# Optimization experiments

Hardware: AMD Instinct MI355X
Metric: run time of the kernel (lower is better)

## Reference

```python
import jax, jax.numpy as jnp
import numpy as np


def setup_inputs() -> dict:
    key = jax.random.key(0)
    ks = jax.random.split(key, 5)
    B, S, E, H, D = 4, 2048, 1024, 16, 64
    sc = 1.0 / np.sqrt(E)
    x = jax.random.normal(ks[0], (B, S, E), dtype=jnp.float32)
    Wq = jax.random.normal(ks[1], (H, E, D), dtype=jnp.float32) * sc
    Wk = jax.random.normal(ks[2], (H, E, D), dtype=jnp.float32) * sc
    Wv = jax.random.normal(ks[3], (H, E, D), dtype=jnp.float32) * sc
    Wo = jax.random.normal(ks[4], (E, E), dtype=jnp.float32) * sc
    bo = jnp.zeros((E,), dtype=jnp.float32)
    return {"x": x, "Wq": Wq, "Wk": Wk, "Wv": Wv, "Wo": Wo, "bo": bo}


def reference(x, Wq, Wk, Wv, Wo, bo):
    # x: [B,S,E]; Wq/Wk/Wv: [H,E,D]; Wo: [E,E]; bo: [E]
    B, S, E = x.shape
    H, _, D = Wq.shape
    q = jnp.einsum('bse,hed->bhsd', x, Wq)
    k = jnp.einsum('bse,hed->bhsd', x, Wk)
    v = jnp.einsum('bse,hed->bhsd', x, Wv)
    scale = jnp.asarray(D, x.dtype) ** -0.5
    att = jnp.einsum('bhsd,bhtd->bhst', q, k) * scale  # [B,H,S,S]
    causal = jnp.tril(jnp.ones((S, S), dtype=bool))
    att = jnp.where(causal, att, jnp.asarray(-jnp.inf, att.dtype))
    att = jax.nn.softmax(att, axis=-1)
    out = jnp.einsum('bhst,bhtd->bhsd', att, v)  # [B,H,S,D]
    # concat heads in order (head dim-major on last axis), then project
    out = out.transpose(0, 2, 1, 3).reshape(B, S, H * D)
    return out @ Wo.T + bo
```

## Files before the change

kernel.cpp:

```cpp
#include <hip/hip_runtime.h>
#include <hip/hip_bf16.h>

#define BB 4
#define SS 2048
#define EE 1024
#define HH 16
#define DD 64
#define MM (BB*SS)
#define HD (HH*DD)
#define NQKV (3*HD)

typedef __bf16 bf16_t;
typedef __bf16 bf16x4 __attribute__((ext_vector_type(4)));
typedef __bf16 bf16x8 __attribute__((ext_vector_type(8)));
typedef float f32x4 __attribute__((ext_vector_type(4)));

#define MFMA16(a,b,c) __builtin_amdgcn_mfma_f32_16x16x32_bf16(a,b,c,0,0,0)
#define NEG_INF (-__builtin_huge_valf())
#define QSCALE 0.1803368801111204f

__device__ __forceinline__ void gload_lds16(const void* g, void* l) {
  __builtin_amdgcn_global_load_lds((const __attribute__((address_space(1))) unsigned int*)g,
                                   (__attribute__((address_space(3))) unsigned int*)l,
                                   16, 0, 0);
}

#define SBAR() __builtin_amdgcn_s_barrier()
#define SCHB() __builtin_amdgcn_sched_barrier(0)
#define VMCNT2 do { asm volatile("s_waitcnt vmcnt(2)" ::: "memory"); } while(0)
#define VMCNT0 do { asm volatile("s_waitcnt vmcnt(0)" ::: "memory"); } while(0)

__global__ __launch_bounds__(256)
void k_f32_to_bf16(const float* __restrict__ in, bf16_t* __restrict__ out, int n8) {
  int i = blockIdx.x*256 + threadIdx.x;
  if (i >= n8) return;
  const float4* p = reinterpret_cast<const float4*>(in) + (size_t)i*2;
  float4 a = p[0], b = p[1];
  bf16x8 o;
  o[0]=(bf16_t)a.x; o[1]=(bf16_t)a.y; o[2]=(bf16_t)a.z; o[3]=(bf16_t)a.w;
  o[4]=(bf16_t)b.x; o[5]=(bf16_t)b.y; o[6]=(bf16_t)b.z; o[7]=(bf16_t)b.w;
  *reinterpret_cast<bf16x8*>(out + (size_t)i*8) = o;
}

__global__ __launch_bounds__(256)
void k_conv_wqkv(const float* __restrict__ Wq, const float* __restrict__ Wk,
                 const float* __restrict__ Wv, bf16_t* __restrict__ Wt) {
  __shared__ float t[64][65];
  int wh = blockIdx.x;
  int which = wh >> 4, h = wh & 15;
  int e0 = blockIdx.y * 64;
  const float* W = (which==0) ? Wq : (which==1) ? Wk : Wv;
  const float* src = W + (size_t)h*EE*DD;
  int r = threadIdx.x >> 6, c = threadIdx.x & 63;
  #pragma unroll
  for (int i = 0; i < 16; ++i) {
    int e = i*4 + r;
    t[e][c] = src[(size_t)(e0+e)*DD + c];
  }
  __syncthreads();
  bf16_t* dst = Wt + (size_t)(which*HD + h*DD)*EE;
  #pragma unroll
  for (int i = 0; i < 16; ++i) {
    int d = i*4 + r;
    dst[(size_t)d*EE + e0 + c] = (bf16_t)t[c][d];
  }
}

#define QK_ITERS 8
template<int EPI, int NTX>
__global__ __launch_bounds__(512, 1)
void k_gemm8(const bf16_t* __restrict__ Ag, const bf16_t* __restrict__ Bg0,
             bf16_t* __restrict__ Qp, bf16_t* __restrict__ Kp, bf16_t* __restrict__ Vtp,
             const float* __restrict__ bias, float* __restrict__ Cout) {
  __shared__ __align__(16) bf16_t Ab[2][128*64];
  __shared__ __align__(16) bf16_t Bb[2][256*64];

  int orig = blockIdx.x;
  int xcd = orig & 7, lidx = orig >> 3;
  int tileY = xcd*8 + (lidx & 7);
  int tileX = lidx >> 3;
  int n0 = tileX * 256, m0 = tileY * 128;

  int tid = threadIdx.x;
  int lane = tid & 63, w = tid >> 6;
  int wr = w >> 2, wc = w & 3;
  int lr = lane & 15, lg = lane >> 4;

  const bf16_t* Bg = Bg0 + (size_t)n0 * EE;

  int r3 = tid >> 3;
  int gch = (tid & 7) ^ (r3 & 7);
  int ldsb = w * 1024;

#define STAGE_A(buf, kt) do { \
    const bf16_t* g_ = Ag + (size_t)(m0 + r3)*EE + (kt)*64 + gch*8; \
    char* l_ = (char*)Ab[buf] + ldsb; \
    gload_lds16(g_, l_); \
    gload_lds16(g_ + (size_t)64*EE, l_ + 8192); \
  } while(0)
#define STAGE_B(buf, kt, half) do { \
    const bf16_t* g_ = Bg + (size_t)((half)*128 + r3)*EE + (kt)*64 + gch*8; \
    char* l_ = (char*)Bb[buf] + (half)*16384 + ldsb; \
    gload_lds16(g_, l_); \
    gload_lds16(g_ + (size_t)64*EE, l_ + 8192); \
  } while(0)

  int sA = lr & 7;
  unsigned aoff[2] = { (unsigned)((wr*64 + lr)*128 + ((lg     ^ sA) << 4)),
                       (unsigned)((wr*64 + lr)*128 + (((4+lg) ^ sA) << 4)) };
  unsigned boff[2] = { (unsigned)((wc*64 + lr)*128 + ((lg     ^ sA) << 4)),
                       (unsigned)((wc*64 + lr)*128 + (((4+lg) ^ sA) << 4)) };

  f32x4 acc[4][4];
  #pragma unroll
  for (int i=0;i<4;i++)
    #pragma unroll
    for (int j=0;j<4;j++) acc[i][j] = (f32x4){0.f,0.f,0.f,0.f};
  bf16x8 af[4], b0, b1;

#define PHASE(buf, kh, nh, WAITV, ...) do { \
    if ((nh) == 0) { \
      _Pragma("unroll") for (int mf_=0; mf_<4; ++mf_) \
        af[mf_] = *reinterpret_cast<const bf16x8*>((const char*)Ab[buf] + aoff[kh] + mf_*2048); \
    } \
    b0 = *reinterpret_cast<const bf16x8*>((const char*)Bb[buf] + boff[kh] + (nh)*4096); \
    b1 = *reinterpret_cast<const bf16x8*>((const char*)Bb[buf] + boff[kh] + (nh)*4096 + 2048); \
    __VA_ARGS__; \
    SBAR(); \
    asm volatile("s_waitcnt lgkmcnt(0)" ::: "memory"); \
    SCHB(); \
    __builtin_amdgcn_s_setprio(1); \
    _Pragma("unroll") for (int mf_=0; mf_<4; ++mf_) { \
      acc[mf_][(nh)*2+0] = MFMA16(af[mf_], b0, acc[mf_][(nh)*2+0]); \
      acc[mf_][(nh)*2+1] = MFMA16(af[mf_], b1, acc[mf_][(nh)*2+1]); } \
    __builtin_amdgcn_s_setprio(0); \
    WAITV; \
    SBAR(); \
    SCHB(); \
  } while(0)

  STAGE_A(0, 0);
  STAGE_B(0, 0, 0); STAGE_B(0, 0, 1);
  STAGE_A(1, 1);
  VMCNT2;
  SBAR();
  SCHB();

#define WAITQ { if (!last) { VMCNT2; } else { VMCNT0; } }
  for (int i = 0; i < QK_ITERS; ++i) {
    int t1 = 2*i+1, t2 = 2*i+2, t3 = 2*i+3;
    bool last = (i == QK_ITERS-1);
    PHASE(0, 0, 0, (void)0, STAGE_B(1, t1, 0));
    PHASE(0, 0, 1, (void)0, STAGE_B(1, t1, 1));
    PHASE(0, 1, 0, (void)0, (void)0);
    PHASE(0, 1, 1, WAITQ,   if (!last) STAGE_A(0, t2));
    PHASE(1, 0, 0, (void)0, if (!last) STAGE_B(0, t2, 0));
    PHASE(1, 0, 1, (void)0, if (!last) STAGE_B(0, t2, 1));
    PHASE(1, 1, 0, (void)0, (void)0);
    PHASE(1, 1, 1, WAITQ,   if (!last) STAGE_A(1, t3));
  }
#undef WAITQ
#undef PHASE
#undef STAGE_A
#undef STAGE_B

  if (EPI == 0) {
    int which = n0 >> 10;
    if (which < 2) {
      #pragma unroll
      for (int mf=0; mf<4; ++mf) {
        #pragma unroll
        for (int nf=0; nf<4; ++nf) {
          int n = n0 + wc*64 + nf*16 + lr;
          int hd = n & 1023, h2 = hd >> 6, d = hd & 63;
          #pragma unroll
          for (int r=0;r<4;r++) {
            int m = m0 + wr*64 + mf*16 + lg*4 + r;
            int b = m >> 11, s = m & 2047;
            size_t bh = (size_t)(b*HH + h2);
            if (which == 0) Qp[(bh*SS + s)*DD + d] = (bf16_t)(acc[mf][nf][r] * QSCALE);
            else            Kp[(bh*SS + s)*DD + d] = (bf16_t)acc[mf][nf][r];
          }
        }
      }
    } else {
      #pragma unroll
      for (int mf=0; mf<4; ++mf) {
        #pragma unroll
        for (int nf=0; nf<4; ++nf) {
          int n = n0 + wc*64 + nf*16 + lr;
          int hd = n & 1023, h2 = hd >> 6, d = hd & 63;
          int m = m0 + wr*64 + mf*16 + lg*4;
          int b = m >> 11, s = m & 2047;
          size_t bh = (size_t)(b*HH + h2);
          bf16x4 vv;
          vv[0] = (bf16_t)acc[mf][nf][0];
          vv[1] = (bf16_t)acc[mf][nf][1];
          vv[2] = (bf16_t)acc[mf][nf][2];
          vv[3] = (bf16_t)acc[mf][nf][3];
          *reinterpret_cast<bf16x4*>(Vtp + (bh*DD + d)*SS + s) = vv;
        }
      }
    }
  } else {
    float bv[4];
    #pragma unroll
    for (int nf=0;nf<4;nf++) bv[nf] = bias[n0 + wc*64 + nf*16 + lr];
    #pragma unroll
    for (int mf=0; mf<4; ++mf)
      #pragma unroll
      for (int nf=0; nf<4; ++nf) {
        int n = n0 + wc*64 + nf*16 + lr;
        #pragma unroll
        for (int r=0;r<4;r++) {
          int m = m0 + wr*64 + mf*16 + lg*4 + r;
          Cout[(size_t)m*HD + n] = acc[mf][nf][r] + bv[nf];
        }
      }
  }
}

__global__ __launch_bounds__(512)
void k_attn(const bf16_t* __restrict__ Q, const bf16_t* __restrict__ K,
            const bf16_t* __restrict__ Vt, bf16_t* __restrict__ AO) {
  __shared__ __align__(16) bf16_t Ks[3][64*64];
  __shared__ __align__(16) bf16_t Vs[3][64*64];

  int id = blockIdx.x;
  int m8 = id & 7, d8 = id >> 3;
  int bh = m8*8 + (d8 >> 3);
  int u  = d8 & 7;

  int tid = threadIdx.x, lane = tid & 63, w = tid >> 6;
  int lr = lane & 15, lg = lane >> 4;
  const bf16_t* Qb = Q  + (size_t)bh * SS * DD;
  const bf16_t* Kp = K  + (size_t)bh * SS * DD;
  const bf16_t* Vp = Vt + (size_t)bh * DD * SS;
  int b = bh >> 4, h = bh & 15;

  int srow = tid >> 3;
  int gchunk = (tid & 7) ^ (srow & 7);

#define STAGE_KV(t, buf) do { \
    int kv0_ = (t)*64; \
    gload_lds16(Kp + (size_t)(kv0_ + srow)*DD + gchunk*8, (char*)Ks[buf] + w*1024); \
    gload_lds16(Vp + (size_t)srow*SS + kv0_ + gchunk*8,   (char*)Vs[buf] + w*1024); \
  } while(0)

  for (int ph = 0; ph < 2; ++ph) {
    int p = ph ? (15 - u) : u;
    int nt = 2*p + 2;
    int qrow0 = p*128 + w*16;
    int q = qrow0 + lr;

    bf16x8 qf[2];
    #pragma unroll
    for (int kk=0;kk<2;kk++)
      qf[kk] = *reinterpret_cast<const bf16x8*>(Qb + (size_t)(qrow0 + lr)*DD + kk*32 + lg*8);

    f32x4 po[4];
    #pragma unroll
    for (int i=0;i<4;i++) po[i] = (f32x4){0.f,0.f,0.f,0.f};
    float accl = 0.f;
    float mrun = NEG_INF;

    STAGE_KV(0, 0);
    STAGE_KV(1, 1);
    for (int t = 0; t < nt; ++t) {
      if (t < nt-1) { VMCNT2; } else { VMCNT0; }
      SBAR();
      SCHB();
      if (t+2 < nt) STAGE_KV(t+2, (t+2)%3);
      int kv0 = t*64;
      if (kv0 > qrow0 + 15) continue;
      int buf = t % 3;
      const bf16_t* Kb = Ks[buf];
      const bf16_t* Vb = Vs[buf];

      f32x4 sa[4];
      #pragma unroll
      for (int ct=0; ct<4; ++ct) {
        int rr = ct*16 + lr;
        int sw = rr & 7;
        bf16x8 k0 = *reinterpret_cast<const bf16x8*>(Kb + rr*64 + ((lg     ^ sw) << 3));
        bf16x8 k1 = *reinterpret_cast<const bf16x8*>(Kb + rr*64 + (((4+lg) ^ sw) << 3));
        f32x4 c = (f32x4){0.f,0.f,0.f,0.f};
        c = MFMA16(k0, qf[0], c);
        c = MFMA16(k1, qf[1], c);
        sa[ct] = c;
      }
      if (kv0 + 63 > qrow0) {
        #pragma unroll
        for (int ct=0;ct<4;ct++) {
          #pragma unroll
          for (int r=0;r<4;r++) {
            int kv = kv0 + ct*16 + lg*4 + r;
            if (kv > q) sa[ct][r] = NEG_INF;
          }
        }
      }
      float v01 = fmaxf(fmaxf(sa[0][0],sa[0][1]), fmaxf(sa[0][2],sa[0][3]));
      float v23 = fmaxf(fmaxf(sa[1][0],sa[1][1]), fmaxf(sa[1][2],sa[1][3]));
      float v45 = fmaxf(fmaxf(sa[2][0],sa[2][1]), fmaxf(sa[2][2],sa[2][3]));
      float v67 = fmaxf(fmaxf(sa[3][0],sa[3][1]), fmaxf(sa[3][2],sa[3][3]));
      float vm = fmaxf(fmaxf(v01,v23), fmaxf(v45,v67));
      vm = fmaxf(vm, __shfl_xor(vm, 16));
      vm = fmaxf(vm, __shfl_xor(vm, 32));
      if (!__all(vm - mrun <= 8.0f)) {
        float mn = fmaxf(mrun, vm);
        float fs = __builtin_amdgcn_exp2f(mrun - mn);
        mrun = mn;
        accl *= fs;
        #pragma unroll
        for (int i=0;i<4;i++) po[i] *= fs;
      }
      bf16x8 pf[2];
      float rs = 0.f;
      #pragma unroll
      for (int ct=0;ct<4;ct++) {
        #pragma unroll
        for (int r=0;r<4;r++) {
          float pv = __builtin_amdgcn_exp2f(sa[ct][r] - mrun);
          rs += pv;
          pf[ct>>1][(ct&1)*4 + r] = (bf16_t)pv;
        }
      }
      rs += __shfl_xor(rs, 16);
      rs += __shfl_xor(rs, 32);
      accl += rs;
      #pragma unroll
      for (int ctd=0; ctd<4; ++ctd) {
        int rr = ctd*16 + lr;
        int sw8 = rr & 7;
        int sub = (lg & 1) << 3;
        const char* rowb = (const char*)Vb + rr*128;
        #pragma unroll
        for (int kk=0; kk<2; ++kk) {
          int c0 = kk*4 + (lg>>1);
          bf16x4 lo = *reinterpret_cast<const bf16x4*>(rowb + (((c0     ^ sw8) << 4) | sub));
          bf16x4 hi = *reinterpret_cast<const bf16x4*>(rowb + ((((c0+2) ^ sw8) << 4) | sub));
          bf16x8 vf;
          vf[0]=lo[0]; vf[1]=lo[1]; vf[2]=lo[2]; vf[3]=lo[3];
          vf[4]=hi[0]; vf[5]=hi[1]; vf[6]=hi[2]; vf[7]=hi[3];
          po[ctd] = MFMA16(vf, pf[kk], po[ctd]);
        }
      }
    }
    SBAR();
    {
      float inv = 1.0f / accl;
      bf16_t* dst = AO + (size_t)(b*SS + q)*HD + h*DD;
      #pragma unroll
      for (int ctd=0;ctd<4;ctd++) {
        bf16x4 vv;
        #pragma unroll
        for (int r=0;r<4;r++) vv[r] = (bf16_t)(po[ctd][r] * inv);
        *reinterpret_cast<bf16x4*>(dst + ctd*16 + lg*4) = vv;
      }
    }
  }
#undef STAGE_KV
}

extern "C" void kernel_launch(void* const* d_in, const int* in_sizes, int n_in,
                              void* d_out, int out_size, void* d_ws, size_t ws_size,
                              hipStream_t stream) {
  const float* x  = (const float*)d_in[0];
  const float* Wq = (const float*)d_in[1];
  const float* Wk = (const float*)d_in[2];
  const float* Wv = (const float*)d_in[3];
  const float* Wo = (const float*)d_in[4];
  const float* bo = (const float*)d_in[5];
  float* out = (float*)d_out;

  char* ws = (char*)d_ws;
  bf16_t* xb  = (bf16_t*)(ws + 0);
  bf16_t* wt  = (bf16_t*)(ws + 16777216);
  bf16_t* wob = (bf16_t*)(ws + 23068672);
  bf16_t* Qb  = (bf16_t*)(ws + 25165824);
  bf16_t* Kb  = (bf16_t*)(ws + 41943040);
  bf16_t* Vtb = (bf16_t*)(ws + 58720256);
  bf16_t* AO  = (bf16_t*)(ws + 75497472);

  k_f32_to_bf16<<<(MM*EE/8)/256, 256, 0, stream>>>(x,  xb,  MM*EE/8);
  k_f32_to_bf16<<<(EE*EE/8)/256, 256, 0, stream>>>(Wo, wob, EE*EE/8);
  dim3 gw(48, 16);
  k_conv_wqkv<<<gw, 256, 0, stream>>>(Wq, Wk, Wv, wt);

  k_gemm8<0,12><<<768, 512, 0, stream>>>(xb, wt, Qb, Kb, Vtb, nullptr, nullptr);

  k_attn<<<BB*HH*8, 512, 0, stream>>>(Qb, Kb, Vtb, AO);

  k_gemm8<1,4><<<256, 512, 0, stream>>>(AO, wob, nullptr, nullptr, nullptr, bo, out);
}
```

Baseline: 182.8 us.

## Process two 16-row Q subtiles per wave in attention with 256-thread blocks

The attention kernel drops from 8 waves of 16 query rows each to 4 waves of 32 query rows each. Each K/V fragment read from LDS now feeds two sets of MFMAs, and every thread issues twice as many global-to-LDS loads per stage. The aim is to halve LDS fragment traffic per FLOP and give more MFMA work between barriers. The cost is more registers per wave, fewer waves per block for hiding latency, and coarser causal skipping, since a wave now skips a tile only when it lies past all 32 of its rows.

```diff
diff --git a/kernel.cpp b/kernel.cpp
--- a/kernel.cpp
+++ b/kernel.cpp
@@ -27,6 +27,7 @@
 
 #define SBAR() __builtin_amdgcn_s_barrier()
 #define SCHB() __builtin_amdgcn_sched_barrier(0)
+#define VMCNT4 do { asm volatile("s_waitcnt vmcnt(4)" ::: "memory"); } while(0)
 #define VMCNT2 do { asm volatile("s_waitcnt vmcnt(2)" ::: "memory"); } while(0)
 #define VMCNT0 do { asm volatile("s_waitcnt vmcnt(0)" ::: "memory"); } while(0)
 
@@ -220,7 +221,7 @@
   }
 }
 
-__global__ __launch_bounds__(512)
+__global__ __launch_bounds__(256)
 void k_attn(const bf16_t* __restrict__ Q, const bf16_t* __restrict__ K,
             const bf16_t* __restrict__ Vt, bf16_t* __restrict__ AO) {
   __shared__ __align__(16) bf16_t Ks[3][64*64];
@@ -238,96 +239,122 @@
   const bf16_t* Vp = Vt + (size_t)bh * DD * SS;
   int b = bh >> 4, h = bh & 15;
 
-  int srow = tid >> 3;
-  int gchunk = (tid & 7) ^ (srow & 7);
+  int r3 = tid >> 3;
+  int gch = (tid & 7) ^ (r3 & 7);
 
 #define STAGE_KV(t, buf) do { \
     int kv0_ = (t)*64; \
-    gload_lds16(Kp + (size_t)(kv0_ + srow)*DD + gchunk*8, (char*)Ks[buf] + w*1024); \
-    gload_lds16(Vp + (size_t)srow*SS + kv0_ + gchunk*8,   (char*)Vs[buf] + w*1024); \
+    const bf16_t* kg_ = Kp + (size_t)(kv0_ + r3)*DD + gch*8; \
+    const bf16_t* vg_ = Vp + (size_t)r3*SS + kv0_ + gch*8; \
+    gload_lds16(kg_,                  (char*)Ks[buf] + w*1024); \
+    gload_lds16(kg_ + (size_t)32*DD,  (char*)Ks[buf] + 4096 + w*1024); \
+    gload_lds16(vg_,                  (char*)Vs[buf] + w*1024); \
+    gload_lds16(vg_ + (size_t)32*SS,  (char*)Vs[buf] + 4096 + w*1024); \
   } while(0)
 
   for (int ph = 0; ph < 2; ++ph) {
     int p = ph ? (15 - u) : u;
     int nt = 2*p + 2;
-    int qrow0 = p*128 + w*16;
-    int q = qrow0 + lr;
-
-    bf16x8 qf[2];
-    #pragma unroll
-    for (int kk=0;kk<2;kk++)
-      qf[kk] = *reinterpret_cast<const bf16x8*>(Qb + (size_t)(qrow0 + lr)*DD + kk*32 + lg*8);
-
-    f32x4 po[4];
-    #pragma unroll
-    for (int i=0;i<4;i++) po[i] = (f32x4){0.f,0.f,0.f,0.f};
-    float accl = 0.f;
-    float mrun = NEG_INF;
+    int qrow0 = p*128 + w*32;
+
+    bf16x8 qf[2][2];
+    #pragma unroll
+    for (int s=0;s<2;s++)
+      #pragma unroll
+      for (int kk=0;kk<2;kk++)
+        qf[s][kk] = *reinterpret_cast<const bf16x8*>(
+            Qb + (size_t)(qrow0 + s*16 + lr)*DD + kk*32 + lg*8);
+
+    f32x4 po[2][4];
+    #pragma unroll
+    for (int s=0;s<2;s++)
+      #pragma unroll
+      for (int i=0;i<4;i++) po[s][i] = (f32x4){0.f,0.f,0.f,0.f};
+    float accl[2] = {0.f, 0.f};
+    float mrun[2] = {NEG_INF, NEG_INF};
 
     STAGE_KV(0, 0);
     STAGE_KV(1, 1);
     for (int t = 0; t < nt; ++t) {
-      if (t < nt-1) { VMCNT2; } else { VMCNT0; }
+      if (t < nt-1) { VMCNT4; } else { VMCNT0; }
       SBAR();
       SCHB();
       if (t+2 < nt) STAGE_KV(t+2, (t+2)%3);
       int kv0 = t*64;
-      if (kv0 > qrow0 + 15) continue;
+      if (kv0 > qrow0 + 31) continue;
       int buf = t % 3;
       const bf16_t* Kb = Ks[buf];
       const bf16_t* Vb = Vs[buf];
 
-      f32x4 sa[4];
+      f32x4 sa[2][4];
       #pragma unroll
       for (int ct=0; ct<4; ++ct) {
         int rr = ct*16 + lr;
         int sw = rr & 7;
         bf16x8 k0 = *reinterpret_cast<const bf16x8*>(Kb + rr*64 + ((lg     ^ sw) << 3));
         bf16x8 k1 = *reinterpret_cast<const bf16x8*>(Kb + rr*64 + (((4+lg) ^ sw) << 3));
-        f32x4 c = (f32x4){0.f,0.f,0.f,0.f};
-        c = MFMA16(k0, qf[0], c);
-        c = MFMA16(k1, qf[1], c);
-        sa[ct] = c;
+        f32x4 c0 = (f32x4){0.f,0.f,0.f,0.f};
+        c0 = MFMA16(k0, qf[0][0], c0);
+        c0 = MFMA16(k1, qf[0][1], c0);
+        sa[0][ct] = c0;
+        f32x4 c1 = (f32x4){0.f,0.f,0.f,0.f};
+        c1 = MFMA16(k0, qf[1][0], c1);
+        c1 = MFMA16(k1, qf[1][1], c1);
+        sa[1][ct] = c1;
       }
       if (kv0 + 63 > qrow0) {
         #pragma unroll
-        for (int ct=0;ct<4;ct++) {
+        for (int s=0;s<2;s++) {
+          int q = qrow0 + s*16 + lr;
+          #pragma unroll
+          for (int ct=0;ct<4;ct++)
+            #pragma unroll
+            for (int r=0;r<4;r++) {
+              int kv = kv0 + ct*16 + lg*4 + r;
+              if (kv > q) sa[s][ct][r] = NEG_INF;
+            }
+        }
+      }
+      float vm[2];
+      #pragma unroll
+      for (int s=0;s<2;s++) {
+        float v01 = fmaxf(fmaxf(sa[s][0][0],sa[s][0][1]), fmaxf(sa[s][0][2],sa[s][0][3]));
+        float v23 = fmaxf(fmaxf(sa[s][1][0],sa[s][1][1]), fmaxf(sa[s][1][2],sa[s][1][3]));
+        float v45 = fmaxf(fmaxf(sa[s][2][0],sa[s][2][1]), fmaxf(sa[s][2][2],sa[s][2][3]));
+        float v67 = fmaxf(fmaxf(sa[s][3][0],sa[s][3][1]), fmaxf(sa[s][3][2],sa[s][3][3]));
+        float v = fmaxf(fmaxf(v01,v23), fmaxf(v45,v67));
+        v = fmaxf(v, __shfl_xor(v, 16));
+        v = fmaxf(v, __shfl_xor(v, 32));
+        vm[s] = v;
+      }
+      float g = fmaxf(vm[0]-mrun[0], vm[1]-mrun[1]);
+      if (!__all(g <= 8.0f)) {
+        #pragma unroll
+        for (int s=0;s<2;s++) {
+          float mn = fmaxf(mrun[s], vm[s]);
+          float fs = __builtin_amdgcn_exp2f(mrun[s] - mn);
+          mrun[s] = mn;
+          accl[s] *= fs;
+          #pragma unroll
+          for (int i=0;i<4;i++) po[s][i] *= fs;
+        }
+      }
+      bf16x8 pf[2][2];
+      #pragma unroll
+      for (int s=0;s<2;s++) {
+        float rs = 0.f;
+        #pragma unroll
+        for (int ct=0;ct<4;ct++)
           #pragma unroll
           for (int r=0;r<4;r++) {
-            int kv = kv0 + ct*16 + lg*4 + r;
-            if (kv > q) sa[ct][r] = NEG_INF;
+            float pv = __builtin_amdgcn_exp2f(sa[s][ct][r] - mrun[s]);
+            rs += pv;
+            pf[s][ct>>1][(ct&1)*4 + r] = (bf16_t)pv;
           }
-        }
-      }
-      float v01 = fmaxf(fmaxf(sa[0][0],sa[0][1]), fmaxf(sa[0][2],sa[0][3]));
-      float v23 = fmaxf(fmaxf(sa[1][0],sa[1][1]), fmaxf(sa[1][2],sa[1][3]));
-      float v45 = fmaxf(fmaxf(sa[2][0],sa[2][1]), fmaxf(sa[2][2],sa[2][3]));
-      float v67 = fmaxf(fmaxf(sa[3][0],sa[3][1]), fmaxf(sa[3][2],sa[3][3]));
-      float vm = fmaxf(fmaxf(v01,v23), fmaxf(v45,v67));
-      vm = fmaxf(vm, __shfl_xor(vm, 16));
-      vm = fmaxf(vm, __shfl_xor(vm, 32));
-      if (!__all(vm - mrun <= 8.0f)) {
-        float mn = fmaxf(mrun, vm);
-        float fs = __builtin_amdgcn_exp2f(mrun - mn);
-        mrun = mn;
-        accl *= fs;
-        #pragma unroll
-        for (int i=0;i<4;i++) po[i] *= fs;
-      }
-      bf16x8 pf[2];
-      float rs = 0.f;
-      #pragma unroll
-      for (int ct=0;ct<4;ct++) {
-        #pragma unroll
-        for (int r=0;r<4;r++) {
-          float pv = __builtin_amdgcn_exp2f(sa[ct][r] - mrun);
-          rs += pv;
-          pf[ct>>1][(ct&1)*4 + r] = (bf16_t)pv;
-        }
-      }
-      rs += __shfl_xor(rs, 16);
-      rs += __shfl_xor(rs, 32);
-      accl += rs;
+        rs += __shfl_xor(rs, 16);
+        rs += __shfl_xor(rs, 32);
+        accl[s] += rs;
+      }
       #pragma unroll
       for (int ctd=0; ctd<4; ++ctd) {
         int rr = ctd*16 + lr;
@@ -342,19 +369,22 @@
           bf16x8 vf;
           vf[0]=lo[0]; vf[1]=lo[1]; vf[2]=lo[2]; vf[3]=lo[3];
           vf[4]=hi[0]; vf[5]=hi[1]; vf[6]=hi[2]; vf[7]=hi[3];
-          po[ctd] = MFMA16(vf, pf[kk], po[ctd]);
+          po[0][ctd] = MFMA16(vf, pf[0][kk], po[0][ctd]);
+          po[1][ctd] = MFMA16(vf, pf[1][kk], po[1][ctd]);
         }
       }
     }
     SBAR();
-    {
-      float inv = 1.0f / accl;
+    #pragma unroll
+    for (int s=0;s<2;s++) {
+      float inv = 1.0f / accl[s];
+      int q = qrow0 + s*16 + lr;
       bf16_t* dst = AO + (size_t)(b*SS + q)*HD + h*DD;
       #pragma unroll
       for (int ctd=0;ctd<4;ctd++) {
         bf16x4 vv;
         #pragma unroll
-        for (int r=0;r<4;r++) vv[r] = (bf16_t)(po[ctd][r] * inv);
+        for (int r=0;r<4;r++) vv[r] = (bf16_t)(po[s][ctd][r] * inv);
         *reinterpret_cast<bf16x4*>(dst + ctd*16 + lg*4) = vv;
       }
     }
@@ -389,7 +419,7 @@
 
   k_gemm8<0,12><<<768, 512, 0, stream>>>(xb, wt, Qb, Kb, Vtb, nullptr, nullptr);
 
-  k_attn<<<BB*HH*8, 512, 0, stream>>>(Qb, Kb, Vtb, AO);
+  k_attn<<<BB*HH*8, 256, 0, stream>>>(Qb, Kb, Vtb, AO);
 
   k_gemm8<1,4><<<256, 512, 0, stream>>>(AO, wob, nullptr, nullptr, nullptr, bo, out);
 }
```

After: 189.4 us. 1.04x slower.
